# Kernel tuning notes

Measured on AMD Instinct MI355X. Metric: run time of the kernel, lower is better.

## Reference

```python
import jax, jax.numpy as jnp
import numpy as np

B = 64; H = 64; W = 64; C = 128
NH = 4; WS = 4; SHIFT = 2
N = WS * WS; HD = C // NH; SCALE = HD ** -0.5
HID = 4 * C; EPS = 1e-6


def _rel_index():
    # faithful to source: meshgrid(coords_w, coords_h, indexing='ij'); hard-coded 4 == WS
    coords = np.stack(np.meshgrid(np.arange(WS), np.arange(WS), indexing='ij')).reshape(2, -1)
    rel = coords[:, :, None] - coords[:, None, :]
    rel = rel.transpose(1, 2, 0).copy()
    rel[:, :, 0] += WS - 1
    rel[:, :, 1] += WS - 1
    rel[:, :, 0] *= 2 * WS - 1
    return rel.sum(-1)  # (N, N) int

REL_IDX = jnp.asarray(_rel_index())


def _attn_mask():
    img = np.zeros((H, W))
    sl = (slice(0, -WS), slice(-WS, -SHIFT), slice(-SHIFT, None))
    cnt = 0
    for hs in sl:
        for ws_ in sl:
            img[hs, ws_] = cnt
            cnt += 1
    mw = img.reshape(H // WS, WS, W // WS, WS).transpose(0, 2, 1, 3).reshape(-1, N)
    m = mw[:, None, :] - mw[:, :, None]  # (nW, N, N)
    return jnp.asarray(np.where(m != 0, -100.0, 0.0).astype(np.float32))

MASK = _attn_mask()  # (nW, N, N)


def _ln(x, s, b):
    mu = x.mean(-1, keepdims=True)
    var = ((x - mu) ** 2).mean(-1, keepdims=True)
    return (x - mu) * jax.lax.rsqrt(var + EPS) * s + b


def setup_inputs() -> dict:
    key = jax.random.key(0)
    ks = jax.random.split(key, 8)
    def nrm(k, shape, scale=0.02):
        return jax.random.normal(k, shape, jnp.float32) * scale
    return dict(
        x=jax.random.normal(ks[0], (B, H * W, C), jnp.float32),
        ln1_scale=jnp.ones((C,), jnp.float32), ln1_bias=jnp.zeros((C,), jnp.float32),
        qkv_w=nrm(ks[1], (C, 3 * C)), qkv_b=jnp.zeros((3 * C,), jnp.float32),
        rel_bias=nrm(ks[2], ((2 * WS - 1) ** 2, NH)),
        proj_w=nrm(ks[3], (C, C)), proj_b=jnp.zeros((C,), jnp.float32),
        ln2_scale=jnp.ones((C,), jnp.float32), ln2_bias=jnp.zeros((C,), jnp.float32),
        fc1_w=nrm(ks[4], (C, HID)), fc1_b=jnp.zeros((HID,), jnp.float32),
        fc2_w=nrm(ks[5], (HID, C)), fc2_b=jnp.zeros((C,), jnp.float32),
    )


def reference(x, ln1_scale, ln1_bias, qkv_w, qkv_b, rel_bias, proj_w, proj_b,
              ln2_scale, ln2_bias, fc1_w, fc1_b, fc2_w, fc2_b):
    shortcut = x
    h = _ln(x, ln1_scale, ln1_bias).reshape(B, H, W, C)
    h = jnp.roll(h, (-SHIFT, -SHIFT), axis=(1, 2))
    # window partition -> (B*nW, N, C)
    xw = h.reshape(B, H // WS, WS, W // WS, WS, C).transpose(0, 1, 3, 2, 4, 5).reshape(-1, N, C)
    B_ = xw.shape[0]
    qkv = (xw @ qkv_w + qkv_b).reshape(B_, N, 3, NH, HD).transpose(2, 0, 3, 1, 4)
    q, k, v = qkv[0] * SCALE, qkv[1], qkv[2]
    attn = jnp.einsum('bhnd,bhmd->bhnm', q, k)  # (B_, NH, N, N)
    bias = rel_bias[REL_IDX.reshape(-1)].reshape(N, N, NH).transpose(2, 0, 1)
    attn = attn + bias[None]
    nW = MASK.shape[0]
    attn = attn.reshape(B_ // nW, nW, NH, N, N) + MASK[None, :, None]
    attn = jax.nn.softmax(attn.reshape(B_, NH, N, N), axis=-1)
    attn = jax.nn.softmax(attn, axis=-1)  # source applies softmax twice when mask is present
    out = jnp.einsum('bhnm,bhmd->bhnd', attn, v).transpose(0, 2, 1, 3).reshape(B_, N, C)
    out = out @ proj_w + proj_b
    # window reverse
    h = out.reshape(B, H // WS, W // WS, WS, WS, C).transpose(0, 1, 3, 2, 4, 5).reshape(B, H, W, C)
    h = jnp.roll(h, (SHIFT, SHIFT), axis=(1, 2)).reshape(B, H * W, C)
    x = shortcut + h
    m = _ln(x, ln2_scale, ln2_bias)
    m = jax.nn.gelu(m @ fc1_w + fc1_b) @ fc2_w + fc2_b  # flax nn.gelu default approximate=True
    return x + m
```

## Files before the change

kernel.cpp:

```cpp
#include <hip/hip_runtime.h>

typedef __bf16 bf16x8 __attribute__((ext_vector_type(8)));
typedef __bf16 bf16x4 __attribute__((ext_vector_type(4)));
typedef float f32x4 __attribute__((ext_vector_type(4)));
typedef unsigned short us8 __attribute__((ext_vector_type(8)));
typedef unsigned short us4 __attribute__((ext_vector_type(4)));
typedef short sh4 __attribute__((ext_vector_type(4)));

#define SCALE_Q 0.17677669529663687f

__device__ __forceinline__ unsigned short f2b(float f) {
    __bf16 h = (__bf16)f;
    return __builtin_bit_cast(unsigned short, h);
}
__device__ __forceinline__ float b2f(unsigned short h) {
    union { unsigned u; float f; } v; v.u = ((unsigned)h) << 16;
    return v.f;
}
__device__ __forceinline__ f32x4 mfma16(us8 a, us8 b, f32x4 c) {
    return __builtin_amdgcn_mfma_f32_16x16x32_bf16(
        __builtin_bit_cast(bf16x8, a), __builtin_bit_cast(bf16x8, b), c, 0, 0, 0);
}

#if __has_builtin(__builtin_amdgcn_mfma_f32_16x16x16bf16_1k)
__device__ __forceinline__ f32x4 mfma16k16(us4 a, us4 b, f32x4 c) {
    return __builtin_amdgcn_mfma_f32_16x16x16bf16_1k(
        __builtin_bit_cast(sh4, a), __builtin_bit_cast(sh4, b), c, 0, 0, 0);
}
#elif __has_builtin(__builtin_amdgcn_mfma_f32_16x16x16_bf16)
__device__ __forceinline__ f32x4 mfma16k16(us4 a, us4 b, f32x4 c) {
    return __builtin_amdgcn_mfma_f32_16x16x16_bf16(
        __builtin_bit_cast(bf16x4, a), __builtin_bit_cast(bf16x4, b), c, 0, 0, 0);
}
#else
__device__ __forceinline__ f32x4 mfma16k16(us4 a, us4 b, f32x4 c) {
    asm volatile("v_mfma_f32_16x16x16_bf16 %0, %1, %2, %0"
                 : "+v"(c) : "v"(a), "v"(b));
    return c;
}
#endif

__device__ __forceinline__ us8 lds_ld8(const unsigned short* base, int byteoff) {
    return *(const us8*)((const char*)base + byteoff);
}
__device__ __forceinline__ void lds_st8(unsigned short* base, int byteoff, us8 v) {
    *(us8*)((char*)base + byteoff) = v;
}

__global__ void k_pack_qkvw(const float* __restrict__ qkv_w, unsigned short* __restrict__ dst) {
    int gid = blockIdx.x * 256 + threadIdx.x;
    int blk = gid >> 9, rem = gid & 511;
    int lane = rem >> 3, j = rem & 7;
    int w = blk / 24, r1 = blk % 24, ct = r1 >> 2, kk = r1 & 3;
    int col = w * 96 + ct * 16 + (lane & 15);
    int k = kk * 32 + (lane >> 4) * 8 + j;
    float v = qkv_w[k * 384 + col];
    if (col < 128) v *= SCALE_Q;
    dst[gid] = f2b(v);
}
__global__ void k_scale_qkvb(const float* __restrict__ qkv_b, float* __restrict__ dst) {
    int i = blockIdx.x * 256 + threadIdx.x;
    if (i < 384) dst[i] = qkv_b[i] * (i < 128 ? SCALE_Q : 1.f);
}
__global__ void k_pack_projw(const float* __restrict__ proj_w, unsigned short* __restrict__ dst) {
    int gid = blockIdx.x * 256 + threadIdx.x;
    int blk = gid >> 9, rem = gid & 511;
    int lane = rem >> 3, j = rem & 7;
    int w = blk >> 3, r1 = blk & 7, ct = r1 >> 2, kk = r1 & 3;
    int col = w * 32 + ct * 16 + (lane & 15);
    int k = kk * 32 + (lane >> 4) * 8 + j;
    dst[gid] = f2b(proj_w[k * 128 + col]);
}

__global__ void k_pack_mlp(const float* __restrict__ fc1_w, const float* __restrict__ fc2_w,
                           unsigned short* __restrict__ wPack) {
    int gid = blockIdx.x * 256 + threadIdx.x;
    int pair = gid >> 13;
    int rem = gid & 8191;
    float v;
    if (rem < 4096) {
        int half = rem >> 11;
        int r2 = rem & 2047;
        int kk = r2 >> 9, r3 = r2 & 511;
        int lane = r3 >> 3, j = r3 & 7;
        int m = lane & 15;
        int col = pair * 32 + (m >> 2) * 8 + half * 4 + (m & 3);
        int k = kk * 32 + (lane >> 4) * 8 + j;
        v = fc1_w[(size_t)k * 512 + col];
    } else {
        int r2 = rem - 4096;
        int co = r2 >> 9, r3 = r2 & 511;
        int lane = r3 >> 3, j = r3 & 7;
        int k = pair * 32 + (lane >> 4) * 8 + j;
        v = fc2_w[(size_t)k * 128 + co * 16 + (lane & 15)];
    }
    wPack[gid] = f2b(v);
}

__global__ __launch_bounds__(256, 3) void k_block1(
    const float* __restrict__ x,
    const float* __restrict__ ln1s, const float* __restrict__ ln1b,
    const unsigned short* __restrict__ qkvWp, const float* __restrict__ qkvBs,
    const float* __restrict__ relb,
    const unsigned short* __restrict__ projWp, const float* __restrict__ projB,
    unsigned short* __restrict__ xmid)
{
    __shared__ unsigned short sm[4 * 6144];
    __shared__ float sbias[196];
    const int tid = threadIdx.x;
    const int wave = tid >> 6, lane = tid & 63;
    const int g = lane >> 4, m16 = lane & 15;
    if (tid < 196) sbias[tid] = relb[tid];
    const int win0 = blockIdx.x * 4;
    const int winM = win0 + wave;
    const int bbM = winM >> 8, whM = (winM >> 4) & 15, wnM = winM & 15;

    {
        float4 sc0 = *(const float4*)(ln1s + m16 * 8);
        float4 sc1 = *(const float4*)(ln1s + m16 * 8 + 4);
        float4 bi0 = *(const float4*)(ln1b + m16 * 8);
        float4 bi1 = *(const float4*)(ln1b + m16 * 8 + 4);
        #pragma unroll
        for (int it = 0; it < 4; ++it) {
            int tok = it * 4 + g;
            int ti = tok >> 2, tj = tok & 3;
            int hh = (whM * 4 + ti + 2) & 63, ww = (wnM * 4 + tj + 2) & 63;
            const float* xr = x + ((((size_t)bbM << 12) | (hh << 6) | ww) * 128) + m16 * 8;
            float4 v0 = *(const float4*)xr, v1 = *(const float4*)(xr + 4);
            float sum = v0.x + v0.y + v0.z + v0.w + v1.x + v1.y + v1.z + v1.w;
            float sq  = v0.x*v0.x + v0.y*v0.y + v0.z*v0.z + v0.w*v0.w
                      + v1.x*v1.x + v1.y*v1.y + v1.z*v1.z + v1.w*v1.w;
            #pragma unroll
            for (int m = 1; m < 16; m <<= 1) { sum += __shfl_xor(sum, m); sq += __shfl_xor(sq, m); }
            float mu = sum * 0.0078125f;
            float rstd = rsqrtf(sq * 0.0078125f - mu * mu + 1e-6f);
            us8 o;
            o[0] = f2b((v0.x - mu) * rstd * sc0.x + bi0.x);
            o[1] = f2b((v0.y - mu) * rstd * sc0.y + bi0.y);
            o[2] = f2b((v0.z - mu) * rstd * sc0.z + bi0.z);
            o[3] = f2b((v0.w - mu) * rstd * sc0.w + bi0.w);
            o[4] = f2b((v1.x - mu) * rstd * sc1.x + bi1.x);
            o[5] = f2b((v1.y - mu) * rstd * sc1.y + bi1.y);
            o[6] = f2b((v1.z - mu) * rstd * sc1.z + bi1.z);
            o[7] = f2b((v1.w - mu) * rstd * sc1.w + bi1.w);
            lds_st8(sm, wave * 12288 + tok * 256 + ((m16 * 16) ^ ((tok & 7) << 4)), o);
        }
    }
    __syncthreads();

    us8 afr[4][4];
    #pragma unroll
    for (int w = 0; w < 4; ++w)
        #pragma unroll
        for (int k = 0; k < 4; ++k)
            afr[w][k] = lds_ld8(sm, w * 12288 + m16 * 256 + ((k * 64 + g * 16) ^ ((m16 & 7) << 4)));
    __syncthreads();

    #pragma unroll
    for (int ct = 0; ct < 6; ++ct) {
        const unsigned short* bp = qkvWp + (size_t)((wave * 6 + ct) * 4) * 512 + lane * 8;
        us8 b0 = *(const us8*)(bp);
        us8 b1 = *(const us8*)(bp + 512);
        us8 b2 = *(const us8*)(bp + 1024);
        us8 b3 = *(const us8*)(bp + 1536);
        f32x4 acc[4] = {{0.f,0.f,0.f,0.f},{0.f,0.f,0.f,0.f},{0.f,0.f,0.f,0.f},{0.f,0.f,0.f,0.f}};
        #pragma unroll
        for (int w = 0; w < 4; ++w) {
            acc[w] = mfma16(afr[w][0], b0, acc[w]);
            acc[w] = mfma16(afr[w][1], b1, acc[w]);
            acc[w] = mfma16(afr[w][2], b2, acc[w]);
            acc[w] = mfma16(afr[w][3], b3, acc[w]);
        }
        const int c = wave * 96 + ct * 16 + m16;
        const float bias = qkvBs[c];
        const int s = c >> 7;
        const int rem = c & 127, hq = rem >> 5, hd = rem & 31;
        #pragma unroll
        for (int w = 0; w < 4; ++w) {
            const int base = w * 12288;
            if (s == 2) {
                us4 pk;
                #pragma unroll
                for (int jj = 0; jj < 4; ++jj) pk[jj] = f2b(acc[w][jj] + bias);
                *(us4*)((char*)sm + base + 8192 + hq * 1024 + hd * 32
                        + ((g ^ ((hd >> 2) & 3)) << 3)) = pk;
            } else {
                #pragma unroll
                for (int jj = 0; jj < 4; ++jj) {
                    int tok = g * 4 + jj;
                    int chunk = (hd >> 3) ^ ((tok >> 1) & 3);
                    *(unsigned short*)((char*)sm + base + s * 4096 + hq * 1024
                                       + tok * 64 + chunk * 16 + (hd & 7) * 2)
                        = f2b(acc[w][jj] + bias);
                }
            }
        }
    }
    __syncthreads();

    {
        const int base = wave * 12288;
        const int ti = m16 >> 2, tj = m16 & 3;
        const int hhq = whM * 4 + ti, wwq = wnM * 4 + tj;
        const int myid = (hhq < 60 ? 0 : (hhq < 62 ? 3 : 6)) + (wwq < 60 ? 0 : (wwq < 62 ? 1 : 2));
        const int qkswz = (g ^ ((m16 >> 1) & 3)) * 16;
        const int vswz  = (g ^ ((m16 >> 2) & 3)) << 3;
        f32x4 po[4][2];
        #pragma unroll
        for (int h = 0; h < 4; ++h) {
            us8 kf = lds_ld8(sm, base + 4096 + h * 1024 + m16 * 64 + qkswz);
            us8 qf = lds_ld8(sm, base +        h * 1024 + m16 * 64 + qkswz);
            f32x4 st = mfma16(kf, qf, (f32x4){0.f,0.f,0.f,0.f});
            float p[4];
            #pragma unroll
            for (int jj = 0; jj < 4; ++jj) {
                int kk = g * 4 + jj;
                int pi = kk >> 2, pj = kk & 3;
                int hhk = whM * 4 + pi, wwk = wnM * 4 + pj;
                int pid = (hhk < 60 ? 0 : (hhk < 62 ? 3 : 6)) + (wwk < 60 ? 0 : (wwk < 62 ? 1 : 2));
                float v = st[jj] + sbias[((ti - pi + 3) * 7 + (tj - pj + 3)) * 4 + h];
                p[jj] = (pid != myid) ? v - 100.f : v;
            }
            #pragma unroll
            for (int rep = 0; rep < 2; ++rep) {
                float mx = fmaxf(fmaxf(p[0], p[1]), fmaxf(p[2], p[3]));
                mx = fmaxf(mx, __shfl_xor(mx, 16));
                mx = fmaxf(mx, __shfl_xor(mx, 32));
                float ssum = 0.f;
                #pragma unroll
                for (int jj = 0; jj < 4; ++jj) { p[jj] = __expf(p[jj] - mx); ssum += p[jj]; }
                ssum += __shfl_xor(ssum, 16);
                ssum += __shfl_xor(ssum, 32);
                float inv = 1.f / ssum;
                #pragma unroll
                for (int jj = 0; jj < 4; ++jj) p[jj] *= inv;
            }
            us4 pf;
            #pragma unroll
            for (int jj = 0; jj < 4; ++jj) pf[jj] = f2b(p[jj]);
            #pragma unroll
            for (int dh = 0; dh < 2; ++dh) {
                us4 vf = *(const us4*)((const char*)sm + base + 8192 + h * 1024
                                       + (dh * 16 + m16) * 32 + vswz);
                po[h][dh] = mfma16k16(vf, pf, (f32x4){0.f,0.f,0.f,0.f});
            }
        }
        #pragma unroll
        for (int h = 0; h < 4; ++h)
            #pragma unroll
            for (int dh = 0; dh < 2; ++dh) {
                us4 pk;
                #pragma unroll
                for (int jj = 0; jj < 4; ++jj) pk[jj] = f2b(po[h][dh][jj]);
                *(us4*)((char*)sm + base + m16 * 256
                        + ((h * 64 + dh * 32 + g * 8) ^ ((m16 & 7) << 4))) = pk;
            }
    }
    __syncthreads();

    {
        us8 cfr[4][4];
        #pragma unroll
        for (int w = 0; w < 4; ++w)
            #pragma unroll
            for (int k = 0; k < 4; ++k)
                cfr[w][k] = lds_ld8(sm, w * 12288 + m16 * 256 + ((k * 64 + g * 16) ^ ((m16 & 7) << 4)));
        #pragma unroll
        for (int ct = 0; ct < 2; ++ct) {
            const unsigned short* bp = projWp + (size_t)((wave * 2 + ct) * 4) * 512 + lane * 8;
            us8 b0 = *(const us8*)(bp);
            us8 b1 = *(const us8*)(bp + 512);
            us8 b2 = *(const us8*)(bp + 1024);
            us8 b3 = *(const us8*)(bp + 1536);
            const int c = wave * 32 + ct * 16 + m16;
            const float pb = projB[c];
            #pragma unroll
            for (int w = 0; w < 4; ++w) {
                f32x4 acc = {0.f, 0.f, 0.f, 0.f};
                acc = mfma16(cfr[w][0], b0, acc);
                acc = mfma16(cfr[w][1], b1, acc);
                acc = mfma16(cfr[w][2], b2, acc);
                acc = mfma16(cfr[w][3], b3, acc);
                const int winw = win0 + w;
                const int bb = winw >> 8, wh = (winw >> 4) & 15, wn = winw & 15;
                #pragma unroll
                for (int jj = 0; jj < 4; ++jj) {
                    int tok = g * 4 + jj;
                    int hh3 = (wh * 4 + (tok >> 2) + 2) & 63;
                    int ww3 = (wn * 4 + (tok & 3) + 2) & 63;
                    size_t t = (((size_t)bb << 12) | (hh3 << 6) | ww3);
                    xmid[t * 128 + c] = f2b(acc[jj] + pb + x[t * 128 + c]);
                }
            }
        }
    }
}

__global__ __launch_bounds__(256, 3) void k_block2(
    const unsigned short* __restrict__ xmid,
    float* __restrict__ out,
    const float* __restrict__ ln2s, const float* __restrict__ ln2b,
    const unsigned short* __restrict__ wPack,
    const float* __restrict__ fc1B, const float* __restrict__ fc2B)
{
    __shared__ unsigned short smem[24576];
    const int tid = threadIdx.x;
    const int wave = tid >> 6, lane = tid & 63;
    const int g = lane >> 4, m16 = lane & 15;
    const size_t r0 = (size_t)blockIdx.x * 128;
    unsigned short* scr = &smem[wave * 2048];

    #pragma unroll
    for (int sub = 0; sub < 4; ++sub) {
        const unsigned short* src = wPack + sub * 2048 + tid * 8;
        unsigned short* dst = &smem[8192 + sub * 2048 + wave * 512];
#if __has_builtin(__builtin_amdgcn_global_load_lds)
        __builtin_amdgcn_global_load_lds(
            (const __attribute__((address_space(1))) void*)src,
            (__attribute__((address_space(3))) void*)dst, 16, 0, 0);
#else
        *(us8*)(dst + lane * 8) = *(const us8*)src;
#endif
    }

    float scv[8], biv[8];
    {
        float4 s0 = *(const float4*)(ln2s + m16 * 8);
        float4 s1 = *(const float4*)(ln2s + m16 * 8 + 4);
        float4 b0 = *(const float4*)(ln2b + m16 * 8);
        float4 b1 = *(const float4*)(ln2b + m16 * 8 + 4);
        scv[0]=s0.x; scv[1]=s0.y; scv[2]=s0.z; scv[3]=s0.w;
        scv[4]=s1.x; scv[5]=s1.y; scv[6]=s1.z; scv[7]=s1.w;
        biv[0]=b0.x; biv[1]=b0.y; biv[2]=b0.z; biv[3]=b0.w;
        biv[4]=b1.x; biv[5]=b1.y; biv[6]=b1.z; biv[7]=b1.w;
    }
    us8 bx[2][4];
    #pragma unroll
    for (int rt = 0; rt < 2; ++rt) {
        #pragma unroll
        for (int it = 0; it < 4; ++it) {
            int lr = it * 4 + g;
            us8 u = *(const us8*)(xmid + (r0 + wave * 32 + rt * 16 + lr) * 128 + m16 * 8);
            float f[8];
            #pragma unroll
            for (int q = 0; q < 8; ++q) f[q] = b2f(u[q]);
            float sum = 0.f, sq = 0.f;
            #pragma unroll
            for (int q = 0; q < 8; ++q) { sum += f[q]; sq += f[q] * f[q]; }
            #pragma unroll
            for (int m = 1; m < 16; m <<= 1) { sum += __shfl_xor(sum, m); sq += __shfl_xor(sq, m); }
            float mu = sum * 0.0078125f;
            float rstd = rsqrtf(sq * 0.0078125f - mu * mu + 1e-6f);
            us8 o;
            #pragma unroll
            for (int q = 0; q < 8; ++q) o[q] = f2b((f[q] - mu) * rstd * scv[q] + biv[q]);
            lds_st8(scr, lr * 256 + ((m16 * 16) ^ ((lr & 7) << 4)), o);
        }
        #pragma unroll
        for (int kk = 0; kk < 4; ++kk)
            bx[rt][kk] = lds_ld8(scr, m16 * 256 + ((kk * 64 + g * 16) ^ ((m16 & 7) << 4)));
    }
    __syncthreads();

    f32x4 accO[2][8];
    #pragma unroll
    for (int rt = 0; rt < 2; ++rt)
        #pragma unroll
        for (int co = 0; co < 8; ++co) accO[rt][co] = (f32x4){0.f, 0.f, 0.f, 0.f};

    for (int p = 0; p < 16; ++p) {
        if (p < 15) {
            #pragma unroll
            for (int sub = 0; sub < 4; ++sub) {
                const unsigned short* src = wPack + (p + 1) * 8192 + sub * 2048 + tid * 8;
                unsigned short* dst = &smem[8192 + ((p + 1) & 1) * 8192 + sub * 2048 + wave * 512];
#if __has_builtin(__builtin_amdgcn_global_load_lds)
                __builtin_amdgcn_global_load_lds(
                    (const __attribute__((address_space(1))) void*)src,
                    (__attribute__((address_space(3))) void*)dst, 16, 0, 0);
#else
                *(us8*)(dst + lane * 8) = *(const us8*)src;
#endif
            }
        }
        const char* wb = (const char*)&smem[8192 + (p & 1) * 8192];
        f32x4 hA0 = {0.f,0.f,0.f,0.f}, hA1 = {0.f,0.f,0.f,0.f};
        #pragma unroll
        for (int kk = 0; kk < 4; ++kk) {
            us8 aw = *(const us8*)(wb + kk * 1024 + lane * 16);
            hA0 = mfma16(aw, bx[0][kk], hA0);
            hA1 = mfma16(aw, bx[1][kk], hA1);
        }
        f32x4 hB0 = {0.f,0.f,0.f,0.f}, hB1 = {0.f,0.f,0.f,0.f};
        #pragma unroll
        for (int kk = 0; kk < 4; ++kk) {
            us8 aw = *(const us8*)(wb + 4096 + kk * 1024 + lane * 16);
            hB0 = mfma16(aw, bx[0][kk], hB0);
            hB1 = mfma16(aw, bx[1][kk], hB1);
        }
        float4 bA = *(const float4*)(fc1B + p * 32 + g * 8);
        float4 bB = *(const float4*)(fc1B + p * 32 + g * 8 + 4);
        us8 pa0, pa1;
        #pragma unroll
        for (int jj = 0; jj < 4; ++jj) {
            float v0 = hA0[jj] + ((const float*)&bA)[jj];
            float z0 = v0 + 0.044715f * v0 * v0 * v0;
            pa0[jj] = f2b(v0 * __builtin_amdgcn_rcpf(1.f + __builtin_amdgcn_exp2f(-2.3022082f * z0)));
            float w0 = hB0[jj] + ((const float*)&bB)[jj];
            float y0 = w0 + 0.044715f * w0 * w0 * w0;
            pa0[4 + jj] = f2b(w0 * __builtin_amdgcn_rcpf(1.f + __builtin_amdgcn_exp2f(-2.3022082f * y0)));
            float v1 = hA1[jj] + ((const float*)&bA)[jj];
            float z1 = v1 + 0.044715f * v1 * v1 * v1;
            pa1[jj] = f2b(v1 * __builtin_amdgcn_rcpf(1.f + __builtin_amdgcn_exp2f(-2.3022082f * z1)));
            float w1 = hB1[jj] + ((const float*)&bB)[jj];
            float y1 = w1 + 0.044715f * w1 * w1 * w1;
            pa1[4 + jj] = f2b(w1 * __builtin_amdgcn_rcpf(1.f + __builtin_amdgcn_exp2f(-2.3022082f * y1)));
        }
        #pragma unroll
        for (int co = 0; co < 8; ++co) {
            us8 bw = *(const us8*)(wb + 8192 + co * 1024 + lane * 16);
            accO[0][co] = mfma16(pa0, bw, accO[0][co]);
            accO[1][co] = mfma16(pa1, bw, accO[1][co]);
        }
        __syncthreads();
    }

    #pragma unroll
    for (int rt = 0; rt < 2; ++rt)
        #pragma unroll
        for (int co = 0; co < 8; ++co) {
            int col = co * 16 + m16;
            float b2v = fc2B[col];
            #pragma unroll
            for (int jj = 0; jj < 4; ++jj) {
                size_t row = r0 + wave * 32 + rt * 16 + g * 4 + jj;
                out[row * 128 + col] = accO[rt][co][jj] + b2v + b2f(xmid[row * 128 + col]);
            }
        }
}

extern "C" void kernel_launch(void* const* d_in, const int* in_sizes, int n_in,
                              void* d_out, int out_size, void* d_ws, size_t ws_size,
                              hipStream_t stream) {
    const float* x        = (const float*)d_in[0];
    const float* ln1_s    = (const float*)d_in[1];
    const float* ln1_b    = (const float*)d_in[2];
    const float* qkv_w    = (const float*)d_in[3];
    const float* qkv_b    = (const float*)d_in[4];
    const float* rel_bias = (const float*)d_in[5];
    const float* proj_w   = (const float*)d_in[6];
    const float* proj_b   = (const float*)d_in[7];
    const float* ln2_s    = (const float*)d_in[8];
    const float* ln2_b    = (const float*)d_in[9];
    const float* fc1_w    = (const float*)d_in[10];
    const float* fc1_b    = (const float*)d_in[11];
    const float* fc2_w    = (const float*)d_in[12];
    const float* fc2_b    = (const float*)d_in[13];
    float* out = (float*)d_out;
    char* ws = (char*)d_ws;

    unsigned short* qkv_wp  = (unsigned short*)(ws);
    unsigned short* proj_wp = (unsigned short*)(ws + 98304);
    unsigned short* wpack   = (unsigned short*)(ws + 131072);
    float*          qkv_bs  = (float*)(ws + 393216);
    unsigned short* xmid    = (unsigned short*)(ws + 524288);

    k_pack_qkvw<<<192, 256, 0, stream>>>(qkv_w, qkv_wp);
    k_scale_qkvb<<<2, 256, 0, stream>>>(qkv_b, qkv_bs);
    k_pack_projw<<<64, 256, 0, stream>>>(proj_w, proj_wp);
    k_pack_mlp<<<512, 256, 0, stream>>>(fc1_w, fc2_w, wpack);

    k_block1<<<4096, 256, 0, stream>>>(x, ln1_s, ln1_b, qkv_wp, qkv_bs, rel_bias,
                                       proj_wp, proj_b, xmid);
    k_block2<<<2048, 256, 0, stream>>>(xmid, out, ln2_s, ln2_b, wpack, fc1_b, fc2_b);
}
```

Measured before the change: 207.2 us.

## Make each wave own one window end-to-end, removing block barriers

Restructures the attention block kernel so each wave computes the full QKV and projection GEMMs for its own window, instead of splitting output columns across waves and sharing windows through LDS. This removes three block-wide __syncthreads and the cross-wave LDS exchange of A fragments. The weight-pack kernels change layout to match. In exchange, each wave now loads all weight tiles from global/L2 (4x more weight traffic per block), and the 24-iteration QKV loop is not unrolled.

```diff
diff --git a/kernel.cpp b/kernel.cpp
--- a/kernel.cpp
+++ b/kernel.cpp
@@ -51,8 +51,8 @@
     int gid = blockIdx.x * 256 + threadIdx.x;
     int blk = gid >> 9, rem = gid & 511;
     int lane = rem >> 3, j = rem & 7;
-    int w = blk / 24, r1 = blk % 24, ct = r1 >> 2, kk = r1 & 3;
-    int col = w * 96 + ct * 16 + (lane & 15);
+    int cc = blk >> 2, kk = blk & 3;
+    int col = cc * 16 + (lane & 15);
     int k = kk * 32 + (lane >> 4) * 8 + j;
     float v = qkv_w[k * 384 + col];
     if (col < 128) v *= SCALE_Q;
@@ -66,8 +66,8 @@
     int gid = blockIdx.x * 256 + threadIdx.x;
     int blk = gid >> 9, rem = gid & 511;
     int lane = rem >> 3, j = rem & 7;
-    int w = blk >> 3, r1 = blk & 7, ct = r1 >> 2, kk = r1 & 3;
-    int col = w * 32 + ct * 16 + (lane & 15);
+    int cc = blk >> 2, kk = blk & 3;
+    int col = cc * 16 + (lane & 15);
     int k = kk * 32 + (lane >> 4) * 8 + j;
     dst[gid] = f2b(proj_w[k * 128 + col]);
 }
@@ -111,9 +111,10 @@
     const int wave = tid >> 6, lane = tid & 63;
     const int g = lane >> 4, m16 = lane & 15;
     if (tid < 196) sbias[tid] = relb[tid];
-    const int win0 = blockIdx.x * 4;
-    const int winM = win0 + wave;
-    const int bbM = winM >> 8, whM = (winM >> 4) & 15, wnM = winM & 15;
+    __syncthreads();
+    const int win = blockIdx.x * 4 + wave;
+    const int bb = win >> 8, wh = (win >> 4) & 15, wn = win & 15;
+    const int base = wave * 12288;
 
     {
         float4 sc0 = *(const float4*)(ln1s + m16 * 8);
@@ -124,8 +125,8 @@
         for (int it = 0; it < 4; ++it) {
             int tok = it * 4 + g;
             int ti = tok >> 2, tj = tok & 3;
-            int hh = (whM * 4 + ti + 2) & 63, ww = (wnM * 4 + tj + 2) & 63;
-            const float* xr = x + ((((size_t)bbM << 12) | (hh << 6) | ww) * 128) + m16 * 8;
+            int hh = (wh * 4 + ti + 2) & 63, ww = (wn * 4 + tj + 2) & 63;
+            const float* xr = x + ((((size_t)bb << 12) | (hh << 6) | ww) * 128) + m16 * 8;
             float4 v0 = *(const float4*)xr, v1 = *(const float4*)(xr + 4);
             float sum = v0.x + v0.y + v0.z + v0.w + v1.x + v1.y + v1.z + v1.w;
             float sq  = v0.x*v0.x + v0.y*v0.y + v0.z*v0.z + v0.w*v0.w
@@ -143,65 +144,51 @@
             o[5] = f2b((v1.y - mu) * rstd * sc1.y + bi1.y);
             o[6] = f2b((v1.z - mu) * rstd * sc1.z + bi1.z);
             o[7] = f2b((v1.w - mu) * rstd * sc1.w + bi1.w);
-            lds_st8(sm, wave * 12288 + tok * 256 + ((m16 * 16) ^ ((tok & 7) << 4)), o);
-        }
-    }
-    __syncthreads();
-
-    us8 afr[4][4];
+            lds_st8(sm, base + tok * 256 + ((m16 * 16) ^ ((tok & 7) << 4)), o);
+        }
+    }
+
+    us8 afr[4];
     #pragma unroll
-    for (int w = 0; w < 4; ++w)
-        #pragma unroll
-        for (int k = 0; k < 4; ++k)
-            afr[w][k] = lds_ld8(sm, w * 12288 + m16 * 256 + ((k * 64 + g * 16) ^ ((m16 & 7) << 4)));
-    __syncthreads();
-
-    #pragma unroll
-    for (int ct = 0; ct < 6; ++ct) {
-        const unsigned short* bp = qkvWp + (size_t)((wave * 6 + ct) * 4) * 512 + lane * 8;
+    for (int k = 0; k < 4; ++k)
+        afr[k] = lds_ld8(sm, base + m16 * 256 + ((k * 64 + g * 16) ^ ((m16 & 7) << 4)));
+
+    for (int cc = 0; cc < 24; ++cc) {
+        const unsigned short* bp = qkvWp + (size_t)(cc * 4) * 512 + lane * 8;
         us8 b0 = *(const us8*)(bp);
         us8 b1 = *(const us8*)(bp + 512);
         us8 b2 = *(const us8*)(bp + 1024);
         us8 b3 = *(const us8*)(bp + 1536);
-        f32x4 acc[4] = {{0.f,0.f,0.f,0.f},{0.f,0.f,0.f,0.f},{0.f,0.f,0.f,0.f},{0.f,0.f,0.f,0.f}};
-        #pragma unroll
-        for (int w = 0; w < 4; ++w) {
-            acc[w] = mfma16(afr[w][0], b0, acc[w]);
-            acc[w] = mfma16(afr[w][1], b1, acc[w]);
-            acc[w] = mfma16(afr[w][2], b2, acc[w]);
-            acc[w] = mfma16(afr[w][3], b3, acc[w]);
-        }
-        const int c = wave * 96 + ct * 16 + m16;
+        f32x4 acc = {0.f, 0.f, 0.f, 0.f};
+        acc = mfma16(afr[0], b0, acc);
+        acc = mfma16(afr[1], b1, acc);
+        acc = mfma16(afr[2], b2, acc);
+        acc = mfma16(afr[3], b3, acc);
+        const int c = cc * 16 + m16;
         const float bias = qkvBs[c];
-        const int s = c >> 7;
+        const int s = cc >> 3;
         const int rem = c & 127, hq = rem >> 5, hd = rem & 31;
-        #pragma unroll
-        for (int w = 0; w < 4; ++w) {
-            const int base = w * 12288;
-            if (s == 2) {
-                us4 pk;
-                #pragma unroll
-                for (int jj = 0; jj < 4; ++jj) pk[jj] = f2b(acc[w][jj] + bias);
-                *(us4*)((char*)sm + base + 8192 + hq * 1024 + hd * 32
-                        + ((g ^ ((hd >> 2) & 3)) << 3)) = pk;
-            } else {
-                #pragma unroll
-                for (int jj = 0; jj < 4; ++jj) {
-                    int tok = g * 4 + jj;
-                    int chunk = (hd >> 3) ^ ((tok >> 1) & 3);
-                    *(unsigned short*)((char*)sm + base + s * 4096 + hq * 1024
-                                       + tok * 64 + chunk * 16 + (hd & 7) * 2)
-                        = f2b(acc[w][jj] + bias);
-                }
-            }
-        }
-    }
-    __syncthreads();
+        if (s == 2) {
+            us4 pk;
+            #pragma unroll
+            for (int jj = 0; jj < 4; ++jj) pk[jj] = f2b(acc[jj] + bias);
+            *(us4*)((char*)sm + base + 8192 + hq * 1024 + hd * 32
+                    + ((g ^ ((hd >> 2) & 3)) << 3)) = pk;
+        } else {
+            #pragma unroll
+            for (int jj = 0; jj < 4; ++jj) {
+                int tok = g * 4 + jj;
+                int chunk = (hd >> 3) ^ ((tok >> 1) & 3);
+                *(unsigned short*)((char*)sm + base + s * 4096 + hq * 1024
+                                   + tok * 64 + chunk * 16 + (hd & 7) * 2)
+                    = f2b(acc[jj] + bias);
+            }
+        }
+    }
 
     {
-        const int base = wave * 12288;
         const int ti = m16 >> 2, tj = m16 & 3;
-        const int hhq = whM * 4 + ti, wwq = wnM * 4 + tj;
+        const int hhq = wh * 4 + ti, wwq = wn * 4 + tj;
         const int myid = (hhq < 60 ? 0 : (hhq < 62 ? 3 : 6)) + (wwq < 60 ? 0 : (wwq < 62 ? 1 : 2));
         const int qkswz = (g ^ ((m16 >> 1) & 3)) * 16;
         const int vswz  = (g ^ ((m16 >> 2) & 3)) << 3;
@@ -216,7 +203,7 @@
             for (int jj = 0; jj < 4; ++jj) {
                 int kk = g * 4 + jj;
                 int pi = kk >> 2, pj = kk & 3;
-                int hhk = whM * 4 + pi, wwk = wnM * 4 + pj;
+                int hhk = wh * 4 + pi, wwk = wn * 4 + pj;
                 int pid = (hhk < 60 ? 0 : (hhk < 62 ? 3 : 6)) + (wwk < 60 ? 0 : (wwk < 62 ? 1 : 2));
                 float v = st[jj] + sbias[((ti - pi + 3) * 7 + (tj - pj + 3)) * 4 + h];
                 p[jj] = (pid != myid) ? v - 100.f : v;
@@ -256,41 +243,33 @@
                         + ((h * 64 + dh * 32 + g * 8) ^ ((m16 & 7) << 4))) = pk;
             }
     }
-    __syncthreads();
 
     {
-        us8 cfr[4][4];
-        #pragma unroll
-        for (int w = 0; w < 4; ++w)
-            #pragma unroll
-            for (int k = 0; k < 4; ++k)
-                cfr[w][k] = lds_ld8(sm, w * 12288 + m16 * 256 + ((k * 64 + g * 16) ^ ((m16 & 7) << 4)));
-        #pragma unroll
-        for (int ct = 0; ct < 2; ++ct) {
-            const unsigned short* bp = projWp + (size_t)((wave * 2 + ct) * 4) * 512 + lane * 8;
+        us8 cfr[4];
+        #pragma unroll
+        for (int k = 0; k < 4; ++k)
+            cfr[k] = lds_ld8(sm, base + m16 * 256 + ((k * 64 + g * 16) ^ ((m16 & 7) << 4)));
+        #pragma unroll
+        for (int cc = 0; cc < 8; ++cc) {
+            const unsigned short* bp = projWp + (size_t)(cc * 4) * 512 + lane * 8;
             us8 b0 = *(const us8*)(bp);
             us8 b1 = *(const us8*)(bp + 512);
             us8 b2 = *(const us8*)(bp + 1024);
             us8 b3 = *(const us8*)(bp + 1536);
-            const int c = wave * 32 + ct * 16 + m16;
+            const int c = cc * 16 + m16;
             const float pb = projB[c];
-            #pragma unroll
-            for (int w = 0; w < 4; ++w) {
-                f32x4 acc = {0.f, 0.f, 0.f, 0.f};
-                acc = mfma16(cfr[w][0], b0, acc);
-                acc = mfma16(cfr[w][1], b1, acc);
-                acc = mfma16(cfr[w][2], b2, acc);
-                acc = mfma16(cfr[w][3], b3, acc);
-                const int winw = win0 + w;
-                const int bb = winw >> 8, wh = (winw >> 4) & 15, wn = winw & 15;
-                #pragma unroll
-                for (int jj = 0; jj < 4; ++jj) {
-                    int tok = g * 4 + jj;
-                    int hh3 = (wh * 4 + (tok >> 2) + 2) & 63;
-                    int ww3 = (wn * 4 + (tok & 3) + 2) & 63;
-                    size_t t = (((size_t)bb << 12) | (hh3 << 6) | ww3);
-                    xmid[t * 128 + c] = f2b(acc[jj] + pb + x[t * 128 + c]);
-                }
+            f32x4 acc = {0.f, 0.f, 0.f, 0.f};
+            acc = mfma16(cfr[0], b0, acc);
+            acc = mfma16(cfr[1], b1, acc);
+            acc = mfma16(cfr[2], b2, acc);
+            acc = mfma16(cfr[3], b3, acc);
+            #pragma unroll
+            for (int jj = 0; jj < 4; ++jj) {
+                int tok = g * 4 + jj;
+                int hh3 = (wh * 4 + (tok >> 2) + 2) & 63;
+                int ww3 = (wn * 4 + (tok & 3) + 2) & 63;
+                size_t t = (((size_t)bb << 12) | (hh3 << 6) | ww3);
+                xmid[t * 128 + c] = f2b(acc[jj] + pb + x[t * 128 + c]);
             }
         }
     }
```

After: 228.8 us. 1.1x slower.
